# Performance work log

Measured on AMD Instinct MI355X. Metric: run time of the kernel, lower is better.

Reference implementation:

```python
import jax, jax.numpy as jnp
import numpy as np

B, S, H, A, F, NCATE, VOCAB, EMB, NCONT = 64, 1024, 512, 256, 2048, 4, 1000, 64, 4


def _layernorm(x, g, b, eps=1e-5):
    m = jnp.mean(x, axis=-1, keepdims=True)
    v = jnp.mean((x - m) ** 2, axis=-1, keepdims=True)
    return (x - m) * jax.lax.rsqrt(v + eps) * g + b


def _positional_encoding(seq_len, d, base=10000.0):
    pos = jnp.arange(seq_len, dtype=jnp.float32)[:, None]
    i = jnp.arange(0, d, 2, dtype=jnp.float32)[None, :]
    ang = pos / jnp.power(base, i / d)
    pe = jnp.zeros((seq_len, d), dtype=jnp.float32)
    pe = pe.at[:, 0::2].set(jnp.sin(ang))
    pe = pe.at[:, 1::2].set(jnp.cos(ang))
    return pe


def setup_inputs() -> dict:
    key = jax.random.key(0)
    ks = jax.random.split(key, 24)
    s = lambda i, shape, fan: jax.random.normal(ks[i], shape, jnp.float32) / np.sqrt(fan)
    inp = {
        'cate_x': jax.random.randint(ks[0], (B, S, NCATE), 0, VOCAB, jnp.int32),
        'cont_x': jax.random.normal(ks[1], (B, S, NCONT), jnp.float32),
        'mask': (jax.random.uniform(ks[2], (B, S)) < 0.9).astype(jnp.float32),
        'targets': jax.random.uniform(ks[3], (B, S), jnp.float32),
        'E_cate': s(4, (NCATE, VOCAB, EMB), EMB),
        'W_proj': s(5, (NCATE * EMB + NCONT, H), NCATE * EMB + NCONT),
        'WQ1': s(6, (H, A), H), 'WK1': s(7, (H, A), H), 'WV1': s(8, (H, A), H),
        'WQ2': s(9, (H, A), H), 'WK2': s(10, (H, A), H), 'WV2': s(11, (H, A), H),
        'W0': s(12, (2 * A, H), 2 * A),
        'ln1_g': jnp.ones((H,), jnp.float32), 'ln1_b': jnp.zeros((H,), jnp.float32),
        'Wf1': s(13, (H, F), H), 'bf1': jnp.zeros((F,), jnp.float32),
        'Wf2': s(14, (F, H), F), 'bf2': jnp.zeros((H,), jnp.float32),
        'ln2_g': jnp.ones((H,), jnp.float32), 'ln2_b': jnp.zeros((H,), jnp.float32),
        'Wfin': s(15, (H, 1), H), 'bfin': jnp.zeros((1,), jnp.float32),
    }
    return inp


def _attn_branch(x, WQ, WK, WV, mask_bias):
    Q = x @ WQ  # [B,S,A]
    K = x @ WK
    V = x @ WV
    scores = jnp.einsum('bsa,bta->bst', Q, K) / np.sqrt(A)
    scores = scores + mask_bias  # additive key-mask [B,1,S]
    return jnp.einsum('bst,bta->bsa', jax.nn.softmax(scores, axis=-1), V)


def reference(cate_x, cont_x, mask, targets, E_cate, W_proj, WQ1, WK1, WV1,
              WQ2, WK2, WV2, W0, ln1_g, ln1_b, Wf1, bf1, Wf2, bf2, ln2_g,
              ln2_b, Wfin, bfin):
    # embedding: per-feature lookup, concat with continuous, project to hidden
    emb = jax.vmap(lambda tab, idx: tab[idx], in_axes=(0, 2), out_axes=2)(E_cate, cate_x)
    emb = emb.reshape(B, S, NCATE * EMB)
    x = jnp.concatenate([emb, cont_x], axis=-1) @ W_proj  # [B,S,H]
    x = x + _positional_encoding(S, H)[None]
    mask_bias = (mask * 1e6 - 1e6)[:, None, :]  # [B,1,S]
    z1 = _attn_branch(x, WQ1, WK1, WV1, mask_bias)
    z2 = _attn_branch(x, WQ2, WK2, WV2, mask_bias)
    z = jnp.concatenate([z1, z2], axis=-1) @ W0
    z = _layernorm(x + z, ln1_g, ln1_b)
    fz = jax.nn.relu(z @ Wf1 + bf1) @ Wf2 + bf2
    z3 = _layernorm(z + fz, ln2_g, ln2_b)
    out = (z3 @ Wfin + bfin).squeeze(-1)  # [B,S]
    return out
```

## Files before the change

### kernel.cpp

```cpp
#include <hip/hip_runtime.h>

typedef unsigned short ushort_t;
typedef unsigned int uint32;
typedef float f32x4 __attribute__((ext_vector_type(4)));
typedef short bf16x8 __attribute__((ext_vector_type(8)));

__device__ __forceinline__ float bf2f(short u) {
  union { uint32 u32; float f; } cv;
  cv.u32 = ((uint32)(ushort_t)u) << 16;
  return cv.f;
}
__device__ __forceinline__ ushort_t f2bf(float f) {
  union { float f; uint32 u; } cv; cv.f = f;
  return (ushort_t)((cv.u + 0x7fffu + ((cv.u >> 16) & 1u)) >> 16);
}
__device__ __forceinline__ uint32 pack2bf(float lo, float hi) {
  return (uint32)f2bf(lo) | ((uint32)f2bf(hi) << 16);
}
__device__ __forceinline__ f32x4 mfma16(bf16x8 a, bf16x8 b, f32x4 c) {
  return __builtin_amdgcn_mfma_f32_16x16x32_bf16(a, b, c, 0, 0, 0);
}
__device__ __forceinline__ void gld_lds16(const ushort_t* g, ushort_t* l) {
  __builtin_amdgcn_global_load_lds(
      (const __attribute__((address_space(1))) void*)g,
      (__attribute__((address_space(3))) void*)l, 16, 0, 0);
}

__global__ __launch_bounds__(256)
void transpose_w(const float* __restrict__ W, ushort_t* __restrict__ WT, int K, int N) {
  __shared__ float s[32][33];
  const int tx = threadIdx.x & 31, ty = threadIdx.x >> 5;
  const int k0 = blockIdx.x * 32, n0 = blockIdx.y * 32;
#pragma unroll
  for (int i = 0; i < 4; ++i)
    s[ty + i * 8][tx] = W[(size_t)(k0 + ty + i * 8) * N + n0 + tx];
  __syncthreads();
#pragma unroll
  for (int i = 0; i < 4; ++i)
    WT[(size_t)(n0 + ty + i * 8) * K + k0 + tx] = f2bf(s[tx][ty + i * 8]);
}

__global__ __launch_bounds__(256)
void ep_kernel(const float* __restrict__ E, const float* __restrict__ Wp,
               ushort_t* __restrict__ EP) {
  const int cv = blockIdx.x;
  const int c = cv / 1000;
  __shared__ float se[64];
  if (threadIdx.x < 64) se[threadIdx.x] = E[(size_t)cv * 64 + threadIdx.x];
  __syncthreads();
  const float* wrow = Wp + (size_t)c * 64 * 512;
  for (int h = threadIdx.x; h < 512; h += 256) {
    float acc = 0.f;
#pragma unroll
    for (int e = 0; e < 64; ++e) acc += se[e] * wrow[(size_t)e * 512 + h];
    EP[(size_t)cv * 512 + h] = f2bf(acc);
  }
}

__global__ __launch_bounds__(256)
void pe_kernel(float* __restrict__ PE) {
  const int id = blockIdx.x * 256 + threadIdx.x;
  const int s = id >> 8, i = id & 255;
  const float ang = (float)s * exp2f(-(float)i * (13.287712379549449f / 256.0f));
  PE[(size_t)s * 512 + 2 * i] = sinf(ang);
  PE[(size_t)s * 512 + 2 * i + 1] = cosf(ang);
}

__global__ __launch_bounds__(256)
void x_kernel(const int* __restrict__ cate, const float* __restrict__ cont,
              const float* __restrict__ Wp, const ushort_t* __restrict__ EP,
              const float* __restrict__ PE, ushort_t* __restrict__ X) {
  const int tid = threadIdx.x;
  const size_t r = (size_t)blockIdx.x * 4 + (tid >> 6);
  const int lane = tid & 63;
  const int h0 = lane * 8;
  const int s = (int)(r & 1023);
  float acc[8];
  const float4 p0 = *(const float4*)(PE + (size_t)s * 512 + h0);
  const float4 p1 = *(const float4*)(PE + (size_t)s * 512 + h0 + 4);
  acc[0] = p0.x; acc[1] = p0.y; acc[2] = p0.z; acc[3] = p0.w;
  acc[4] = p1.x; acc[5] = p1.y; acc[6] = p1.z; acc[7] = p1.w;
#pragma unroll
  for (int c = 0; c < 4; ++c) {
    const int idx = cate[r * 4 + c];
    const bf16x8 e8 = *(const bf16x8*)(EP + ((size_t)(c * 1000 + idx)) * 512 + h0);
#pragma unroll
    for (int k = 0; k < 8; ++k) acc[k] += bf2f(e8[k]);
  }
#pragma unroll
  for (int j = 0; j < 4; ++j) {
    const float cj = cont[r * 4 + j];
    const float4 w0 = *(const float4*)(Wp + (size_t)(256 + j) * 512 + h0);
    const float4 w1 = *(const float4*)(Wp + (size_t)(256 + j) * 512 + h0 + 4);
    acc[0] += cj * w0.x; acc[1] += cj * w0.y; acc[2] += cj * w0.z; acc[3] += cj * w0.w;
    acc[4] += cj * w1.x; acc[5] += cj * w1.y; acc[6] += cj * w1.z; acc[7] += cj * w1.w;
  }
  bf16x8 ov;
#pragma unroll
  for (int k = 0; k < 8; ++k) ov[k] = (short)f2bf(acc[k]);
  *(bf16x8*)(X + r * 512 + h0) = ov;
}

template <int EPI, bool TSTORE>
__global__ __launch_bounds__(256, 2)
void gemm_bt(const ushort_t* __restrict__ A, const ushort_t* __restrict__ BT,
             ushort_t* __restrict__ C, const float* __restrict__ bias, int N, int K) {
  __shared__ __align__(16) ushort_t sA[128 * 64];
  __shared__ __align__(16) ushort_t sB[128 * 64];
  const int tid = threadIdx.x;
  const int lane = tid & 63;
  const int wid = tid >> 6;
  const int l15 = lane & 15, l4 = lane >> 4;
  const int wr = (wid >> 1) * 64, wc = (wid & 1) * 64;
  const size_t rowA0 = (size_t)blockIdx.x * 128;
  const size_t rowB0 = (size_t)blockIdx.y * 128;

  f32x4 acc[4][4] = {};

  for (int kt = 0; kt < K; kt += 64) {
#pragma unroll
    for (int it = 0; it < 4; ++it) {
      const int L = it * 256 + tid;
      const int row = L >> 3;
      const int c = (L & 7) ^ (row & 7);
      gld_lds16(A + (rowA0 + row) * K + kt + c * 8, sA + (size_t)L * 8);
      gld_lds16(BT + (rowB0 + row) * K + kt + c * 8, sB + (size_t)L * 8);
    }
    __syncthreads();
#pragma unroll
    for (int kk = 0; kk < 2; ++kk) {
      bf16x8 af[4], bfr[4];
#pragma unroll
      for (int mi = 0; mi < 4; ++mi) {
        const int row = wr + mi * 16 + l15;
        const int c = (kk * 4 + l4) ^ (row & 7);
        af[mi] = *(const bf16x8*)(sA + row * 64 + c * 8);
      }
#pragma unroll
      for (int ni = 0; ni < 4; ++ni) {
        const int row = wc + ni * 16 + l15;
        const int c = (kk * 4 + l4) ^ (row & 7);
        bfr[ni] = *(const bf16x8*)(sB + row * 64 + c * 8);
      }
#pragma unroll
      for (int mi = 0; mi < 4; ++mi)
#pragma unroll
        for (int ni = 0; ni < 4; ++ni)
          acc[mi][ni] = mfma16(af[mi], bfr[ni], acc[mi][ni]);
    }
    __syncthreads();
  }
#pragma unroll
  for (int ni = 0; ni < 4; ++ni) {
    const int col = (int)rowB0 + wc + ni * 16 + l15;
    float bv = 0.f;
    if (EPI > 0) bv = bias[col];
#pragma unroll
    for (int mi = 0; mi < 4; ++mi) {
      const size_t row0 = rowA0 + wr + mi * 16 + l4 * 4;
      if (TSTORE) {
        ushort4 ov;
        ov.x = f2bf(acc[mi][ni][0]);
        ov.y = f2bf(acc[mi][ni][1]);
        ov.z = f2bf(acc[mi][ni][2]);
        ov.w = f2bf(acc[mi][ni][3]);
        *(ushort4*)(C + ((row0 >> 10) * 256 + (size_t)col) * 1024 + (row0 & 1023)) = ov;
      } else {
#pragma unroll
        for (int j = 0; j < 4; ++j) {
          float v = acc[mi][ni][j] + bv;
          if (EPI == 2) v = fmaxf(v, 0.f);
          C[(row0 + j) * N + col] = f2bf(v);
        }
      }
    }
  }
}

__global__ __launch_bounds__(256, 2)
void attn_kernel(const ushort_t* __restrict__ Q, const ushort_t* __restrict__ Kb,
                 const ushort_t* __restrict__ VT, const float* __restrict__ mask,
                 ushort_t* __restrict__ Z, int colOff) {
  __shared__ __align__(16) ushort_t sK[64 * 256];
  __shared__ __align__(16) ushort_t sV[256 * 64];
  const int tid = threadIdx.x, lane = tid & 63, w = tid >> 6;
  const int l15 = lane & 15, l4 = lane >> 4;
  const int id = blockIdx.x;
  const int b = ((id >> 7) << 3) | (id & 7);
  const int qb = (id >> 3) & 15;
  const int q0 = qb * 64 + w * 16;

  bf16x8 qf[8];
  {
    const ushort_t* qrow = Q + ((size_t)b * 1024 + q0 + l15) * 256;
#pragma unroll
    for (int kk = 0; kk < 8; ++kk)
      qf[kk] = *(const bf16x8*)(qrow + kk * 32 + l4 * 8);
  }
  float m_run = -3.0e38f, l_run = 0.f;
  f32x4 o[16] = {};
  const int src0 = ((l4 & 1) << 5) + l15;
  const bool hiSel = (l4 >= 2);

  for (int t0 = 0; t0 < 1024; t0 += 64) {
#pragma unroll
    for (int it = 0; it < 8; ++it) {
      const int L = it * 256 + tid;
      const int rk = L >> 5;
      const int ck = (L & 24) | ((L ^ rk) & 7);
      gld_lds16(Kb + ((size_t)b * 1024 + t0 + rk) * 256 + ck * 8, sK + (size_t)L * 8);
      const int rv = L >> 3;
      const int cv2 = (L ^ rv) & 7;
      gld_lds16(VT + ((size_t)b * 256 + rv) * 1024 + t0 + cv2 * 8, sV + (size_t)L * 8);
    }
    __syncthreads();

    f32x4 st[4] = {};
#pragma unroll
    for (int fi = 0; fi < 4; ++fi) {
      const int row = fi * 16 + l15;
      const ushort_t* kr = sK + row * 256;
#pragma unroll
      for (int kk = 0; kk < 8; ++kk) {
        const int c = kk * 4 + l4;
        const int cs = (c & 24) | ((c ^ row) & 7);
        const bf16x8 kf = *(const bf16x8*)(kr + cs * 8);
        st[fi] = mfma16(kf, qf[kk], st[fi]);
      }
    }

    float pr[4][4];
    float tmax = -3.0e38f;
#pragma unroll
    for (int fi = 0; fi < 4; ++fi) {
      const float4 mk = *(const float4*)(mask + (size_t)b * 1024 + t0 + fi * 16 + l4 * 4);
      pr[fi][0] = st[fi][0] * 0.0625f + (mk.x * 1e6f - 1e6f);
      pr[fi][1] = st[fi][1] * 0.0625f + (mk.y * 1e6f - 1e6f);
      pr[fi][2] = st[fi][2] * 0.0625f + (mk.z * 1e6f - 1e6f);
      pr[fi][3] = st[fi][3] * 0.0625f + (mk.w * 1e6f - 1e6f);
      tmax = fmaxf(tmax, fmaxf(fmaxf(pr[fi][0], pr[fi][1]), fmaxf(pr[fi][2], pr[fi][3])));
    }
    tmax = fmaxf(tmax, __shfl_xor(tmax, 16));
    tmax = fmaxf(tmax, __shfl_xor(tmax, 32));

    if (!__all(tmax <= m_run + 8.f)) {
      const float m_new = fmaxf(m_run, tmax);
      const float alpha = __expf(m_run - m_new);
      l_run *= alpha;
      m_run = m_new;
#pragma unroll
      for (int ai = 0; ai < 16; ++ai) o[ai] *= alpha;
    }

    float rs = 0.f;
#pragma unroll
    for (int fi = 0; fi < 4; ++fi)
#pragma unroll
      for (int j = 0; j < 4; ++j) {
        pr[fi][j] = __expf(pr[fi][j] - m_run);
        rs += pr[fi][j];
      }
    rs += __shfl_xor(rs, 16);
    rs += __shfl_xor(rs, 32);
    l_run += rs;

    uint32 pk[4][2];
#pragma unroll
    for (int fi = 0; fi < 4; ++fi) {
      pk[fi][0] = pack2bf(pr[fi][0], pr[fi][1]);
      pk[fi][1] = pack2bf(pr[fi][2], pr[fi][3]);
    }
    bf16x8 pf[2];
#pragma unroll
    for (int kk2 = 0; kk2 < 2; ++kk2) {
      const uint32 a0 = __shfl(pk[2 * kk2][0], src0);
      const uint32 a1 = __shfl(pk[2 * kk2][1], src0);
      const uint32 a2 = __shfl(pk[2 * kk2][0], src0 + 16);
      const uint32 a3 = __shfl(pk[2 * kk2][1], src0 + 16);
      const uint32 b0 = __shfl(pk[2 * kk2 + 1][0], src0);
      const uint32 b1 = __shfl(pk[2 * kk2 + 1][1], src0);
      const uint32 b2 = __shfl(pk[2 * kk2 + 1][0], src0 + 16);
      const uint32 b3 = __shfl(pk[2 * kk2 + 1][1], src0 + 16);
      uint4 wv;
      wv.x = hiSel ? b0 : a0;
      wv.y = hiSel ? b1 : a1;
      wv.z = hiSel ? b2 : a2;
      wv.w = hiSel ? b3 : a3;
      pf[kk2] = __builtin_bit_cast(bf16x8, wv);
    }

#pragma unroll
    for (int ai = 0; ai < 16; ++ai) {
      const int row = ai * 16 + l15;
      const ushort_t* vr = sV + row * 64;
#pragma unroll
      for (int kk2 = 0; kk2 < 2; ++kk2) {
        const int c = (kk2 * 4 + l4) ^ (row & 7);
        const bf16x8 vf = *(const bf16x8*)(vr + c * 8);
        o[ai] = mfma16(vf, pf[kk2], o[ai]);
      }
    }
    __syncthreads();
  }

  const float inv = 1.f / l_run;
  const size_t zrow = ((size_t)b * 1024 + q0 + l15) * 512;
#pragma unroll
  for (int ai = 0; ai < 16; ++ai) {
    ushort4 ov;
    ov.x = f2bf(o[ai][0] * inv);
    ov.y = f2bf(o[ai][1] * inv);
    ov.z = f2bf(o[ai][2] * inv);
    ov.w = f2bf(o[ai][3] * inv);
    *(ushort4*)(Z + zrow + colOff + ai * 16 + l4 * 4) = ov;
  }
}

__global__ __launch_bounds__(256)
void ln_kernel(const ushort_t* __restrict__ Xa, const ushort_t* __restrict__ Xb2,
               const float* __restrict__ g, const float* __restrict__ bb,
               ushort_t* __restrict__ O) {
  const int tid = threadIdx.x;
  const size_t r = (size_t)blockIdx.x * 4 + (tid >> 6);
  const int lane = tid & 63;
  const int h0 = lane * 8;
  const bf16x8 va = *(const bf16x8*)(Xa + r * 512 + h0);
  const bf16x8 vb = *(const bf16x8*)(Xb2 + r * 512 + h0);
  float v[8], s1 = 0.f, s2 = 0.f;
#pragma unroll
  for (int k = 0; k < 8; ++k) {
    v[k] = bf2f(va[k]) + bf2f(vb[k]);
    s1 += v[k];
    s2 += v[k] * v[k];
  }
#pragma unroll
  for (int m = 1; m < 64; m <<= 1) {
    s1 += __shfl_xor(s1, m);
    s2 += __shfl_xor(s2, m);
  }
  const float mean = s1 * (1.f / 512.f);
  const float var = s2 * (1.f / 512.f) - mean * mean;
  const float rstd = rsqrtf(var + 1e-5f);
  const float4 g0 = *(const float4*)(g + h0);
  const float4 g1 = *(const float4*)(g + h0 + 4);
  const float4 b0 = *(const float4*)(bb + h0);
  const float4 b1 = *(const float4*)(bb + h0 + 4);
  const float gg[8] = {g0.x, g0.y, g0.z, g0.w, g1.x, g1.y, g1.z, g1.w};
  const float bbv[8] = {b0.x, b0.y, b0.z, b0.w, b1.x, b1.y, b1.z, b1.w};
  bf16x8 ov;
#pragma unroll
  for (int k = 0; k < 8; ++k)
    ov[k] = (short)f2bf((v[k] - mean) * rstd * gg[k] + bbv[k]);
  *(bf16x8*)(O + r * 512 + h0) = ov;
}

__global__ __launch_bounds__(256)
void ln_fin_kernel(const ushort_t* __restrict__ Xa, const ushort_t* __restrict__ Xb2,
                   const float* __restrict__ g, const float* __restrict__ bb,
                   const float* __restrict__ Wfin, const float* __restrict__ bfin,
                   float* __restrict__ out) {
  const int tid = threadIdx.x;
  const size_t r = (size_t)blockIdx.x * 4 + (tid >> 6);
  const int lane = tid & 63;
  const int h0 = lane * 8;
  const bf16x8 va = *(const bf16x8*)(Xa + r * 512 + h0);
  const bf16x8 vb = *(const bf16x8*)(Xb2 + r * 512 + h0);
  float v[8], s1 = 0.f, s2 = 0.f;
#pragma unroll
  for (int k = 0; k < 8; ++k) {
    v[k] = bf2f(va[k]) + bf2f(vb[k]);
    s1 += v[k];
    s2 += v[k] * v[k];
  }
#pragma unroll
  for (int m = 1; m < 64; m <<= 1) {
    s1 += __shfl_xor(s1, m);
    s2 += __shfl_xor(s2, m);
  }
  const float mean = s1 * (1.f / 512.f);
  const float var = s2 * (1.f / 512.f) - mean * mean;
  const float rstd = rsqrtf(var + 1e-5f);
  const float4 g0 = *(const float4*)(g + h0);
  const float4 g1 = *(const float4*)(g + h0 + 4);
  const float4 b0 = *(const float4*)(bb + h0);
  const float4 b1 = *(const float4*)(bb + h0 + 4);
  const float4 w0 = *(const float4*)(Wfin + h0);
  const float4 w1 = *(const float4*)(Wfin + h0 + 4);
  const float gg[8] = {g0.x, g0.y, g0.z, g0.w, g1.x, g1.y, g1.z, g1.w};
  const float bbv[8] = {b0.x, b0.y, b0.z, b0.w, b1.x, b1.y, b1.z, b1.w};
  const float ww[8] = {w0.x, w0.y, w0.z, w0.w, w1.x, w1.y, w1.z, w1.w};
  float dot = 0.f;
#pragma unroll
  for (int k = 0; k < 8; ++k)
    dot += ((v[k] - mean) * rstd * gg[k] + bbv[k]) * ww[k];
#pragma unroll
  for (int m = 1; m < 64; m <<= 1) dot += __shfl_xor(dot, m);
  if (lane == 0) out[r] = dot + bfin[0];
}

extern "C" void kernel_launch(void* const* d_in, const int* in_sizes, int n_in,
                              void* d_out, int out_size, void* d_ws, size_t ws_size,
                              hipStream_t stream) {
  (void)in_sizes; (void)n_in; (void)out_size; (void)ws_size;
  const int* cate   = (const int*)d_in[0];
  const float* cont = (const float*)d_in[1];
  const float* mask = (const float*)d_in[2];
  const float* E    = (const float*)d_in[4];
  const float* Wp   = (const float*)d_in[5];
  const float* WQ1  = (const float*)d_in[6];
  const float* WK1  = (const float*)d_in[7];
  const float* WV1  = (const float*)d_in[8];
  const float* WQ2  = (const float*)d_in[9];
  const float* WK2  = (const float*)d_in[10];
  const float* WV2  = (const float*)d_in[11];
  const float* W0   = (const float*)d_in[12];
  const float* ln1g = (const float*)d_in[13];
  const float* ln1b = (const float*)d_in[14];
  const float* Wf1  = (const float*)d_in[15];
  const float* bf1  = (const float*)d_in[16];
  const float* Wf2  = (const float*)d_in[17];
  const float* bf2  = (const float*)d_in[18];
  const float* ln2g = (const float*)d_in[19];
  const float* ln2b = (const float*)d_in[20];
  const float* Wfin = (const float*)d_in[21];
  const float* bfin = (const float*)d_in[22];
  float* out = (float*)d_out;
  char* ws = (char*)d_ws;

  const size_t MB = 1ull << 20;
  ushort_t* Xb  = (ushort_t*)(ws + 0);
  ushort_t* Qb  = (ushort_t*)(ws + 64 * MB);
  ushort_t* Kb  = (ushort_t*)(ws + 96 * MB);
  ushort_t* VTb = (ushort_t*)(ws + 128 * MB);
  ushort_t* Zb  = (ushort_t*)(ws + 160 * MB);
  ushort_t* T0b = (ushort_t*)(ws + 64 * MB);
  ushort_t* H1b = (ushort_t*)(ws + 128 * MB);
  ushort_t* Gb  = (ushort_t*)(ws + 0);
  ushort_t* T1b = (ushort_t*)(ws + 64 * MB);
  const size_t OW = 224 * MB;
  ushort_t* wq1t = (ushort_t*)(ws + OW + 0);
  ushort_t* wk1t = (ushort_t*)(ws + OW + 262144);
  ushort_t* wv1t = (ushort_t*)(ws + OW + 524288);
  ushort_t* wq2t = (ushort_t*)(ws + OW + 786432);
  ushort_t* wk2t = (ushort_t*)(ws + OW + 1048576);
  ushort_t* wv2t = (ushort_t*)(ws + OW + 1310720);
  ushort_t* w0t  = (ushort_t*)(ws + OW + 1572864);
  ushort_t* wf1t = (ushort_t*)(ws + OW + 2097152);
  ushort_t* wf2t = (ushort_t*)(ws + OW + 4194304);
  ushort_t* epb  = (ushort_t*)(ws + OW + 6291456);
  float*    peb  = (float*)   (ws + OW + 10485760);

  const dim3 blk(256);
  transpose_w<<<dim3(16, 8), blk, 0, stream>>>(WQ1, wq1t, 512, 256);
  transpose_w<<<dim3(16, 8), blk, 0, stream>>>(WK1, wk1t, 512, 256);
  transpose_w<<<dim3(16, 8), blk, 0, stream>>>(WV1, wv1t, 512, 256);
  transpose_w<<<dim3(16, 8), blk, 0, stream>>>(WQ2, wq2t, 512, 256);
  transpose_w<<<dim3(16, 8), blk, 0, stream>>>(WK2, wk2t, 512, 256);
  transpose_w<<<dim3(16, 8), blk, 0, stream>>>(WV2, wv2t, 512, 256);
  transpose_w<<<dim3(16, 16), blk, 0, stream>>>(W0, w0t, 512, 512);
  transpose_w<<<dim3(16, 64), blk, 0, stream>>>(Wf1, wf1t, 512, 2048);
  transpose_w<<<dim3(64, 16), blk, 0, stream>>>(Wf2, wf2t, 2048, 512);
  ep_kernel<<<4000, blk, 0, stream>>>(E, Wp, epb);
  pe_kernel<<<1024, blk, 0, stream>>>(peb);
  x_kernel<<<16384, blk, 0, stream>>>(cate, cont, Wp, epb, peb, Xb);
  gemm_bt<0, false><<<dim3(512, 2), blk, 0, stream>>>(Xb, wq1t, Qb, nullptr, 256, 512);
  gemm_bt<0, false><<<dim3(512, 2), blk, 0, stream>>>(Xb, wk1t, Kb, nullptr, 256, 512);
  gemm_bt<0, true><<<dim3(512, 2), blk, 0, stream>>>(Xb, wv1t, VTb, nullptr, 256, 512);
  attn_kernel<<<dim3(1024), blk, 0, stream>>>(Qb, Kb, VTb, mask, Zb, 0);
  gemm_bt<0, false><<<dim3(512, 2), blk, 0, stream>>>(Xb, wq2t, Qb, nullptr, 256, 512);
  gemm_bt<0, false><<<dim3(512, 2), blk, 0, stream>>>(Xb, wk2t, Kb, nullptr, 256, 512);
  gemm_bt<0, true><<<dim3(512, 2), blk, 0, stream>>>(Xb, wv2t, VTb, nullptr, 256, 512);
  attn_kernel<<<dim3(1024), blk, 0, stream>>>(Qb, Kb, VTb, mask, Zb, 256);
  gemm_bt<0, false><<<dim3(512, 4), blk, 0, stream>>>(Zb, w0t, T0b, nullptr, 512, 512);
  ln_kernel<<<16384, blk, 0, stream>>>(Xb, T0b, ln1g, ln1b, H1b);
  for (int rc = 0; rc < 4; ++rc) {
    const ushort_t* h1c = H1b + (size_t)rc * 16384 * 512;
    ushort_t* t1c = T1b + (size_t)rc * 16384 * 512;
    gemm_bt<2, false><<<dim3(128, 16), blk, 0, stream>>>(h1c, wf1t, Gb, bf1, 2048, 512);
    gemm_bt<1, false><<<dim3(128, 4), blk, 0, stream>>>(Gb, wf2t, t1c, bf2, 512, 2048);
  }
  ln_fin_kernel<<<16384, blk, 0, stream>>>(H1b, T1b, ln2g, ln2b, Wfin, bfin, out);
}
```

Before: 1.009 ms.

## Batch weight transposes into one launch, raise GEMM occupancy, prioritize attention MFMA

Replaces the nine separate weight-transpose launches with a single kernel that picks its source and destination matrix from the block index, cutting launch overhead. It also raises the GEMM launch-bounds occupancy hint from 2 to 3 blocks per CU, and wraps the attention MFMA loops in s_setprio to raise wave priority during matrix work. The occupancy change may force register spilling in the GEMM. The priority hints only reorder issue between waves and may have little effect.

```diff
diff --git a/kernel.cpp b/kernel.cpp
--- a/kernel.cpp
+++ b/kernel.cpp
@@ -26,18 +26,37 @@
       (__attribute__((address_space(3))) void*)l, 16, 0, 0);
 }
 
+struct TPtrs {
+  const float* s[9];
+  ushort_t* d[9];
+};
 __global__ __launch_bounds__(256)
-void transpose_w(const float* __restrict__ W, ushort_t* __restrict__ WT, int K, int N) {
-  __shared__ float s[32][33];
+void transpose_all(TPtrs p) {
+  const int id = blockIdx.x;
+  const float* S;
+  ushort_t* D;
+  int K, N, lt;
+  if (id < 768) {
+    const int wsel = id >> 7;
+    lt = id & 127; S = p.s[wsel]; D = p.d[wsel]; K = 512; N = 256;
+  } else if (id < 1024) {
+    lt = id - 768; S = p.s[6]; D = p.d[6]; K = 512; N = 512;
+  } else if (id < 2048) {
+    lt = id - 1024; S = p.s[7]; D = p.d[7]; K = 512; N = 2048;
+  } else {
+    lt = id - 2048; S = p.s[8]; D = p.d[8]; K = 2048; N = 512;
+  }
+  const int ntn = N >> 5;
+  const int k0 = (lt / ntn) * 32, n0 = (lt % ntn) * 32;
+  __shared__ float sm[32][33];
   const int tx = threadIdx.x & 31, ty = threadIdx.x >> 5;
-  const int k0 = blockIdx.x * 32, n0 = blockIdx.y * 32;
 #pragma unroll
   for (int i = 0; i < 4; ++i)
-    s[ty + i * 8][tx] = W[(size_t)(k0 + ty + i * 8) * N + n0 + tx];
+    sm[ty + i * 8][tx] = S[(size_t)(k0 + ty + i * 8) * N + n0 + tx];
   __syncthreads();
 #pragma unroll
   for (int i = 0; i < 4; ++i)
-    WT[(size_t)(n0 + ty + i * 8) * K + k0 + tx] = f2bf(s[tx][ty + i * 8]);
+    D[(size_t)(n0 + ty + i * 8) * K + k0 + tx] = f2bf(sm[tx][ty + i * 8]);
 }
 
 __global__ __launch_bounds__(256)
@@ -102,7 +121,7 @@
 }
 
 template <int EPI, bool TSTORE>
-__global__ __launch_bounds__(256, 2)
+__global__ __launch_bounds__(256, 3)
 void gemm_bt(const ushort_t* __restrict__ A, const ushort_t* __restrict__ BT,
              ushort_t* __restrict__ C, const float* __restrict__ bias, int N, int K) {
   __shared__ __align__(16) ushort_t sA[128 * 64];
@@ -215,6 +234,7 @@
     }
     __syncthreads();
 
+    __builtin_amdgcn_s_setprio(1);
     f32x4 st[4] = {};
 #pragma unroll
     for (int fi = 0; fi < 4; ++fi) {
@@ -228,6 +248,7 @@
         st[fi] = mfma16(kf, qf[kk], st[fi]);
       }
     }
+    __builtin_amdgcn_s_setprio(0);
 
     float pr[4][4];
     float tmax = -3.0e38f;
@@ -289,6 +310,7 @@
       pf[kk2] = __builtin_bit_cast(bf16x8, wv);
     }
 
+    __builtin_amdgcn_s_setprio(1);
 #pragma unroll
     for (int ai = 0; ai < 16; ++ai) {
       const int row = ai * 16 + l15;
@@ -300,6 +322,7 @@
         o[ai] = mfma16(vf, pf[kk2], o[ai]);
       }
     }
+    __builtin_amdgcn_s_setprio(0);
     __syncthreads();
   }
 
@@ -451,15 +474,14 @@
   float*    peb  = (float*)   (ws + OW + 10485760);
 
   const dim3 blk(256);
-  transpose_w<<<dim3(16, 8), blk, 0, stream>>>(WQ1, wq1t, 512, 256);
-  transpose_w<<<dim3(16, 8), blk, 0, stream>>>(WK1, wk1t, 512, 256);
-  transpose_w<<<dim3(16, 8), blk, 0, stream>>>(WV1, wv1t, 512, 256);
-  transpose_w<<<dim3(16, 8), blk, 0, stream>>>(WQ2, wq2t, 512, 256);
-  transpose_w<<<dim3(16, 8), blk, 0, stream>>>(WK2, wk2t, 512, 256);
-  transpose_w<<<dim3(16, 8), blk, 0, stream>>>(WV2, wv2t, 512, 256);
-  transpose_w<<<dim3(16, 16), blk, 0, stream>>>(W0, w0t, 512, 512);
-  transpose_w<<<dim3(16, 64), blk, 0, stream>>>(Wf1, wf1t, 512, 2048);
-  transpose_w<<<dim3(64, 16), blk, 0, stream>>>(Wf2, wf2t, 2048, 512);
+  TPtrs tp;
+  tp.s[0] = WQ1; tp.s[1] = WK1; tp.s[2] = WV1;
+  tp.s[3] = WQ2; tp.s[4] = WK2; tp.s[5] = WV2;
+  tp.s[6] = W0;  tp.s[7] = Wf1; tp.s[8] = Wf2;
+  tp.d[0] = wq1t; tp.d[1] = wk1t; tp.d[2] = wv1t;
+  tp.d[3] = wq2t; tp.d[4] = wk2t; tp.d[5] = wv2t;
+  tp.d[6] = w0t;  tp.d[7] = wf1t; tp.d[8] = wf2t;
+  transpose_all<<<dim3(3072), blk, 0, stream>>>(tp);
   ep_kernel<<<4000, blk, 0, stream>>>(E, Wp, epb);
   pe_kernel<<<1024, blk, 0, stream>>>(peb);
   x_kernel<<<16384, blk, 0, stream>>>(cate, cont, Wp, epb, peb, Xb);
```

Measured after the change: 994.0 us. About the same (-1.5%).
